# Optimization experiments

Measured on AMD Instinct MI355X. Metric: run time of the kernel, lower is better.

Reference implementation:

```python
import jax, jax.numpy as jnp
import numpy as np

R = 32          # voxel resolution
NORMALIZE = True
EPS = 0.0


def setup_inputs() -> dict:
    key = jax.random.key(0)
    k1, k2 = jax.random.split(key)
    B, N, C = 8, 32768, 64
    features = jax.random.normal(k1, (B, N, C), dtype=jnp.float32)
    coords = jax.random.normal(k2, (B, N, 3), dtype=jnp.float32)
    return {"features": features, "coords": coords}


def _norm_coords(coords):
    # coords: (B, N, 3). Faithful to the torch code: mean over dim 2 (xyz),
    # norm over dim 1 (points), max over dim 2.
    nc = coords - coords.mean(axis=2, keepdims=True)
    if NORMALIZE:
        denom = jnp.max(jnp.linalg.norm(nc, axis=1, keepdims=True), axis=2, keepdims=True) * 2.0 + EPS
        nc = nc / denom + 0.5
    else:
        nc = (nc + 1.0) / 2.0
    return jnp.clip(nc * R, 0, R - 1)


def _avg_voxelize(features, vox_coords):
    B, N, C = features.shape
    R3 = R * R * R
    idx = vox_coords[..., 0] * (R * R) + vox_coords[..., 1] * R + vox_coords[..., 2]  # (B, N)
    flat_idx = (jnp.arange(B, dtype=jnp.int32)[:, None] * R3 + idx).reshape(-1)  # (B*N,)
    sums = jax.ops.segment_sum(features.reshape(B * N, C), flat_idx, num_segments=B * R3)
    counts = jax.ops.segment_sum(jnp.ones((B * N, 1), features.dtype), flat_idx, num_segments=B * R3)
    voxf = sums / jnp.maximum(counts, 1.0)              # (B*R3, C)
    voxf = voxf.reshape(B, R, R, R, C).transpose(0, 4, 1, 2, 3)  # (B, C, R, R, R)
    return voxf


def reference(features, coords):
    nc = _norm_coords(jax.lax.stop_gradient(coords))
    vox_coords = jnp.round(nc).astype(jnp.int32)
    return _avg_voxelize(features, vox_coords), nc
```

## Files before the change

kernel.cpp:

```cpp
#include <hip/hip_runtime.h>
#include <math.h>

#define RR 32
#define R3 (RR*RR*RR)
#define BATCH 8
#define NPTS 32768
#define CCH 64

typedef float vfloat4 __attribute__((ext_vector_type(4)));

static constexpr int SB   = 64;
static constexpr int SBT  = SB * BATCH;
static constexpr int VZB  = 1024;
static constexpr int CZB  = 16;
static constexpr int WPB  = 128;
static constexpr int PPW  = NPTS / WPB;
static constexpr int CHUNK = 64;
static constexpr int NCH  = PPW / CHUNK;

static constexpr size_t OFF_COUNTS   = 0;
static constexpr size_t OFF_PARTIALS = 1u << 20;

__global__ __launch_bounds__(256) void prep_kernel(const float* __restrict__ coords,
                                                   float* __restrict__ voxf,
                                                   int* __restrict__ counts,
                                                   float* __restrict__ partials) {
    int bx = blockIdx.x;
    int tid = threadIdx.x;
    if (bx < SBT) {
        int b = bx >> 6, sb = bx & 63;
        const float* cbase = coords + ((size_t)b * NPTS + sb * (NPTS / SB)) * 3;
        float sx = 0.f, sy = 0.f, sz = 0.f;
        #pragma unroll
        for (int k = 0; k < (NPTS / SB) / 256; ++k) {
            const float* p = cbase + (k * 256 + tid) * 3;
            float x = p[0], y = p[1], z = p[2];
            float m = (x + y + z) * (1.0f / 3.0f);
            float dx = x - m, dy = y - m, dz = z - m;
            sx += dx * dx; sy += dy * dy; sz += dz * dz;
        }
        #pragma unroll
        for (int off = 1; off < 64; off <<= 1) {
            sx += __shfl_xor(sx, off);
            sy += __shfl_xor(sy, off);
            sz += __shfl_xor(sz, off);
        }
        __shared__ float ls[3][4];
        int w = tid >> 6;
        if ((tid & 63) == 0) { ls[0][w] = sx; ls[1][w] = sy; ls[2][w] = sz; }
        __syncthreads();
        if (tid == 0) {
            float* o = partials + (size_t)bx * 3;
            o[0] = ls[0][0] + ls[0][1] + ls[0][2] + ls[0][3];
            o[1] = ls[1][0] + ls[1][1] + ls[1][2] + ls[1][3];
            o[2] = ls[2][0] + ls[2][1] + ls[2][2] + ls[2][3];
        }
        return;
    }
    int zb = bx - SBT;
    vfloat4 z = (vfloat4)(0.f);
    if (zb < VZB) {
        vfloat4* o4 = (vfloat4*)voxf + (size_t)zb * 4096;
        #pragma unroll
        for (int k = 0; k < 16; ++k) o4[k * 256 + tid] = z;
    } else {
        vfloat4* c4 = (vfloat4*)counts + (size_t)(zb - VZB) * 4096;
        #pragma unroll
        for (int k = 0; k < 16; ++k) c4[k * 256 + tid] = z;
    }
}

__global__ __launch_bounds__(256) void feat_kernel(const float* __restrict__ features,
                                                   const float* __restrict__ coords,
                                                   const float* __restrict__ partials,
                                                   float* __restrict__ nc_out,
                                                   int* __restrict__ counts,
                                                   float* __restrict__ voxf) {
    int b = blockIdx.y;
    int tid = threadIdx.x;
    int w = blockIdx.x * 4 + (tid >> 6);
    int lane = tid & 63;
    int sub = lane >> 4;
    int cb  = (lane & 15) << 2;
    const float* fbase = features + (size_t)b * NPTS * CCH;
    const float* crd = coords + (size_t)b * NPTS * 3;
    int* cnt = counts + (size_t)b * R3;
    float* obase = voxf + (size_t)b * CCH * R3;
    int p0 = w * PPW;

    float4 fbuf[2][16];
    #pragma unroll
    for (int i = 0; i < 16; ++i)
        fbuf[0][i] = *(const float4*)(fbase + (size_t)(p0 + i * 4 + sub) * CCH + cb);

    const float* ps = partials + ((size_t)b * SB + lane) * 3;
    float qx = ps[0], qy = ps[1], qz = ps[2];
    #pragma unroll
    for (int off = 1; off < 64; off <<= 1) {
        qx += __shfl_xor(qx, off);
        qy += __shfl_xor(qy, off);
        qz += __shfl_xor(qz, off);
    }
    float mx = fmaxf(fmaxf(sqrtf(qx), sqrtf(qy)), sqrtf(qz));
    float rd = 0.5f / mx;

    float4 acc = make_float4(0.f, 0.f, 0.f, 0.f);
    int curv = -1;
    int nrun = 0;

    auto flushRun = [&]() {
        if (curv < 0) return;
        if (lane == 0) atomicAdd(&cnt[curv], nrun);
        float sx = acc.x, sy = acc.y, sz = acc.z, sw = acc.w;
        sx += __shfl_xor(sx, 16); sx += __shfl_xor(sx, 32);
        sy += __shfl_xor(sy, 16); sy += __shfl_xor(sy, 32);
        sz += __shfl_xor(sz, 16); sz += __shfl_xor(sz, 32);
        sw += __shfl_xor(sw, 16); sw += __shfl_xor(sw, 32);
        float val = (sub == 0) ? sx : (sub == 1) ? sy : (sub == 2) ? sz : sw;
        atomicAdd(&obase[(size_t)(cb + sub) * R3 + curv], val);
    };

    #pragma unroll
    for (int c = 0; c < NCH; ++c) {
        int cur = c & 1;
        if (c + 1 < NCH) {
            #pragma unroll
            for (int i = 0; i < 16; ++i)
                fbuf[cur ^ 1][i] = *(const float4*)(fbase +
                    (size_t)(p0 + (c + 1) * CHUNK + i * 4 + sub) * CCH + cb);
        }
        int pp = p0 + c * CHUNK + lane;
        float x = crd[pp * 3], y = crd[pp * 3 + 1], zz = crd[pp * 3 + 2];
        float m = (x + y + zz) * (1.0f / 3.0f);
        float fx = (x - m) * rd + 0.5f;
        float fy = (y - m) * rd + 0.5f;
        float fz = (zz - m) * rd + 0.5f;
        float tx = fminf(fmaxf(fx * (float)RR, 0.0f), (float)(RR - 1));
        float ty = fminf(fmaxf(fy * (float)RR, 0.0f), (float)(RR - 1));
        float tz = fminf(fmaxf(fz * (float)RR, 0.0f), (float)(RR - 1));
        float* onc = nc_out + (size_t)(b * NPTS + pp) * 3;
        onc[0] = tx; onc[1] = ty; onc[2] = tz;
        int v = (int)rintf(tx) * (RR * RR) + (int)rintf(ty) * RR + (int)rintf(tz);

        int v0 = __shfl(v, 0);
        if (__all(v == v0)) {
            if (v0 != curv) {
                flushRun();
                acc = make_float4(0.f, 0.f, 0.f, 0.f);
                nrun = 0;
                curv = v0;
            }
            #pragma unroll
            for (int i = 0; i < 16; ++i) {
                acc.x += fbuf[cur][i].x; acc.y += fbuf[cur][i].y;
                acc.z += fbuf[cur][i].z; acc.w += fbuf[cur][i].w;
            }
            nrun += CHUNK;
        } else {
            flushRun();
            acc = make_float4(0.f, 0.f, 0.f, 0.f);
            nrun = 0;
            curv = -1;
            atomicAdd(&cnt[v], 1);
            #pragma unroll
            for (int i = 0; i < 16; ++i) {
                int vv = __shfl(v, i * 4 + sub);
                size_t o = (size_t)cb * R3 + vv;
                atomicAdd(&obase[o],          fbuf[cur][i].x);
                atomicAdd(&obase[o + R3],     fbuf[cur][i].y);
                atomicAdd(&obase[o + 2 * R3], fbuf[cur][i].z);
                atomicAdd(&obase[o + 3 * R3], fbuf[cur][i].w);
            }
        }
    }
    flushRun();
}

__global__ __launch_bounds__(256) void scale_kernel(const int* __restrict__ counts,
                                                    float* __restrict__ out) {
    int t = blockIdx.x * 256 + threadIdx.x;
    int lane = threadIdx.x & 63;
    int b = t >> 15;
    int vox = t & (R3 - 1);
    int cnt = counts[t];
    unsigned long long mask = __ballot(cnt > 1);
    while (mask) {
        int src = __ffsll((long long)mask) - 1;
        mask &= mask - 1;
        int vv = __shfl(vox, src);
        int bb = __shfl(b, src);
        int cc = __shfl(cnt, src);
        float s = 1.0f / (float)cc;
        size_t o = ((size_t)bb * CCH + lane) * R3 + vv;
        out[o] *= s;
    }
}

extern "C" void kernel_launch(void* const* d_in, const int* in_sizes, int n_in,
                              void* d_out, int out_size, void* d_ws, size_t ws_size,
                              hipStream_t stream) {
    const float* features = (const float*)d_in[0];
    const float* coords   = (const float*)d_in[1];
    float* out = (float*)d_out;

    float* voxf = out;
    float* nc   = out + (size_t)BATCH * CCH * R3;

    char* ws = (char*)d_ws;
    int*   counts   = (int*)(ws + OFF_COUNTS);
    float* partials = (float*)(ws + OFF_PARTIALS);

    prep_kernel<<<SBT + VZB + CZB, 256, 0, stream>>>(coords, voxf, counts, partials);

    dim3 fgrid(WPB / 4, BATCH);
    feat_kernel<<<fgrid, 256, 0, stream>>>(features, coords, partials, nc, counts, voxf);

    scale_kernel<<<BATCH * R3 / 256, 256, 0, stream>>>(counts, voxf);
}
```

Baseline: 31.82 us.

## Precompute voxel indices and counts so feature scatter applies the mean directly

Splits the pipeline into a stats pass, a per-point pass that writes normalized coords, voxel indices and counts while zeroing the output, and a feature scatter that divides by the final count before each atomic add. This removes the separate scale kernel and its read-modify-write over the output volume, and takes the coordinate math off the feature kernel's path. Feature loads become nontemporal. In exchange the scatter now reads counts for every atomic, adds an index buffer round trip, and still needs three launches.

```diff
diff --git a/kernel.cpp b/kernel.cpp
--- a/kernel.cpp
+++ b/kernel.cpp
@@ -11,8 +11,8 @@
 
 static constexpr int SB   = 64;
 static constexpr int SBT  = SB * BATCH;
+static constexpr int CZB  = 16;
 static constexpr int VZB  = 1024;
-static constexpr int CZB  = 16;
 static constexpr int WPB  = 128;
 static constexpr int PPW  = NPTS / WPB;
 static constexpr int CHUNK = 64;
@@ -20,61 +20,107 @@
 
 static constexpr size_t OFF_COUNTS   = 0;
 static constexpr size_t OFF_PARTIALS = 1u << 20;
-
-__global__ __launch_bounds__(256) void prep_kernel(const float* __restrict__ coords,
-                                                   float* __restrict__ voxf,
-                                                   int* __restrict__ counts,
-                                                   float* __restrict__ partials) {
+static constexpr size_t OFF_IDX      = (1u << 20) + (64u << 10);
+
+__global__ __launch_bounds__(256) void stats_kernel(const float* __restrict__ coords,
+                                                    int* __restrict__ counts,
+                                                    float* __restrict__ partials) {
     int bx = blockIdx.x;
     int tid = threadIdx.x;
-    if (bx < SBT) {
-        int b = bx >> 6, sb = bx & 63;
-        const float* cbase = coords + ((size_t)b * NPTS + sb * (NPTS / SB)) * 3;
-        float sx = 0.f, sy = 0.f, sz = 0.f;
-        #pragma unroll
-        for (int k = 0; k < (NPTS / SB) / 256; ++k) {
-            const float* p = cbase + (k * 256 + tid) * 3;
-            float x = p[0], y = p[1], z = p[2];
-            float m = (x + y + z) * (1.0f / 3.0f);
-            float dx = x - m, dy = y - m, dz = z - m;
-            sx += dx * dx; sy += dy * dy; sz += dz * dz;
-        }
-        #pragma unroll
-        for (int off = 1; off < 64; off <<= 1) {
-            sx += __shfl_xor(sx, off);
-            sy += __shfl_xor(sy, off);
-            sz += __shfl_xor(sz, off);
-        }
-        __shared__ float ls[3][4];
-        int w = tid >> 6;
-        if ((tid & 63) == 0) { ls[0][w] = sx; ls[1][w] = sy; ls[2][w] = sz; }
-        __syncthreads();
-        if (tid == 0) {
-            float* o = partials + (size_t)bx * 3;
-            o[0] = ls[0][0] + ls[0][1] + ls[0][2] + ls[0][3];
-            o[1] = ls[1][0] + ls[1][1] + ls[1][2] + ls[1][3];
-            o[2] = ls[2][0] + ls[2][1] + ls[2][2] + ls[2][3];
-        }
-        return;
-    }
-    int zb = bx - SBT;
-    vfloat4 z = (vfloat4)(0.f);
-    if (zb < VZB) {
-        vfloat4* o4 = (vfloat4*)voxf + (size_t)zb * 4096;
-        #pragma unroll
-        for (int k = 0; k < 16; ++k) o4[k * 256 + tid] = z;
-    } else {
-        vfloat4* c4 = (vfloat4*)counts + (size_t)(zb - VZB) * 4096;
+    if (bx >= SBT) {
+        vfloat4 z = (vfloat4)(0.f);
+        vfloat4* c4 = (vfloat4*)counts + (size_t)(bx - SBT) * 4096;
         #pragma unroll
         for (int k = 0; k < 16; ++k) c4[k * 256 + tid] = z;
+        return;
+    }
+    int b = bx >> 6, sb = bx & 63;
+    const float* cbase = coords + ((size_t)b * NPTS + sb * (NPTS / SB)) * 3;
+    float sx = 0.f, sy = 0.f, sz = 0.f;
+    #pragma unroll
+    for (int k = 0; k < (NPTS / SB) / 256; ++k) {
+        const float* p = cbase + (k * 256 + tid) * 3;
+        float x = p[0], y = p[1], z = p[2];
+        float m = (x + y + z) * (1.0f / 3.0f);
+        float dx = x - m, dy = y - m, dz = z - m;
+        sx += dx * dx; sy += dy * dy; sz += dz * dz;
+    }
+    #pragma unroll
+    for (int off = 1; off < 64; off <<= 1) {
+        sx += __shfl_xor(sx, off);
+        sy += __shfl_xor(sy, off);
+        sz += __shfl_xor(sz, off);
+    }
+    __shared__ float ls[3][4];
+    int w = tid >> 6;
+    if ((tid & 63) == 0) { ls[0][w] = sx; ls[1][w] = sy; ls[2][w] = sz; }
+    __syncthreads();
+    if (tid == 0) {
+        float* o = partials + (size_t)bx * 3;
+        o[0] = ls[0][0] + ls[0][1] + ls[0][2] + ls[0][3];
+        o[1] = ls[1][0] + ls[1][1] + ls[1][2] + ls[1][3];
+        o[2] = ls[2][0] + ls[2][1] + ls[2][2] + ls[2][3];
+    }
+}
+
+__global__ __launch_bounds__(256) void points_kernel(const float* __restrict__ coords,
+                                                     const float* __restrict__ partials,
+                                                     float* __restrict__ voxf,
+                                                     float* __restrict__ nc_out,
+                                                     int* __restrict__ idx_out,
+                                                     int* __restrict__ counts) {
+    int bx = blockIdx.x;
+    int tid = threadIdx.x;
+    int gid = bx * 256 + tid;
+    int b = gid >> 15;
+    int lane = tid & 63;
+
+    float x = coords[(size_t)gid * 3];
+    float y = coords[(size_t)gid * 3 + 1];
+    float zz = coords[(size_t)gid * 3 + 2];
+    const float* ps = partials + ((size_t)b * SB + lane) * 3;
+    float qx = ps[0], qy = ps[1], qz = ps[2];
+
+    {
+        vfloat4 z = (vfloat4)(0.f);
+        vfloat4* o4 = (vfloat4*)voxf + (size_t)bx * 4096;
+        #pragma unroll
+        for (int k = 0; k < 16; ++k)
+            __builtin_nontemporal_store(z, &o4[k * 256 + tid]);
+    }
+
+    #pragma unroll
+    for (int off = 1; off < 64; off <<= 1) {
+        qx += __shfl_xor(qx, off);
+        qy += __shfl_xor(qy, off);
+        qz += __shfl_xor(qz, off);
+    }
+    float mx = fmaxf(fmaxf(sqrtf(qx), sqrtf(qy)), sqrtf(qz));
+    float rd = 0.5f / mx;
+
+    float m = (x + y + zz) * (1.0f / 3.0f);
+    float fx = (x - m) * rd + 0.5f;
+    float fy = (y - m) * rd + 0.5f;
+    float fz = (zz - m) * rd + 0.5f;
+    float tx = fminf(fmaxf(fx * (float)RR, 0.0f), (float)(RR - 1));
+    float ty = fminf(fmaxf(fy * (float)RR, 0.0f), (float)(RR - 1));
+    float tz = fminf(fmaxf(fz * (float)RR, 0.0f), (float)(RR - 1));
+    float* onc = nc_out + (size_t)gid * 3;
+    onc[0] = tx; onc[1] = ty; onc[2] = tz;
+    int v = (int)rintf(tx) * (RR * RR) + (int)rintf(ty) * RR + (int)rintf(tz);
+    idx_out[gid] = v;
+
+    int v0 = __shfl(v, 0);
+    if (__all(v == v0)) {
+        if (lane == 0) atomicAdd(&counts[b * R3 + v0], 64);
+    } else {
+        atomicAdd(&counts[b * R3 + v], 1);
     }
 }
 
 __global__ __launch_bounds__(256) void feat_kernel(const float* __restrict__ features,
-                                                   const float* __restrict__ coords,
-                                                   const float* __restrict__ partials,
-                                                   float* __restrict__ nc_out,
-                                                   int* __restrict__ counts,
+                                                   const int* __restrict__ idx,
+                                                   const int* __restrict__ counts,
                                                    float* __restrict__ voxf) {
     int b = blockIdx.y;
     int tid = threadIdx.x;
@@ -83,41 +129,35 @@
     int sub = lane >> 4;
     int cb  = (lane & 15) << 2;
     const float* fbase = features + (size_t)b * NPTS * CCH;
-    const float* crd = coords + (size_t)b * NPTS * 3;
-    int* cnt = counts + (size_t)b * R3;
+    const int* ibase = idx + (size_t)b * NPTS;
+    const int* cnt = counts + (size_t)b * R3;
     float* obase = voxf + (size_t)b * CCH * R3;
     int p0 = w * PPW;
 
-    float4 fbuf[2][16];
+    int vv[NCH];
+    #pragma unroll
+    for (int c = 0; c < NCH; ++c) vv[c] = ibase[p0 + c * CHUNK + lane];
+
+    vfloat4 fbuf[2][16];
     #pragma unroll
     for (int i = 0; i < 16; ++i)
-        fbuf[0][i] = *(const float4*)(fbase + (size_t)(p0 + i * 4 + sub) * CCH + cb);
-
-    const float* ps = partials + ((size_t)b * SB + lane) * 3;
-    float qx = ps[0], qy = ps[1], qz = ps[2];
-    #pragma unroll
-    for (int off = 1; off < 64; off <<= 1) {
-        qx += __shfl_xor(qx, off);
-        qy += __shfl_xor(qy, off);
-        qz += __shfl_xor(qz, off);
-    }
-    float mx = fmaxf(fmaxf(sqrtf(qx), sqrtf(qy)), sqrtf(qz));
-    float rd = 0.5f / mx;
-
-    float4 acc = make_float4(0.f, 0.f, 0.f, 0.f);
+        fbuf[0][i] = __builtin_nontemporal_load(
+            (const vfloat4*)(fbase + (size_t)(p0 + i * 4 + sub) * CCH + cb));
+
+    vfloat4 acc = (vfloat4)(0.f);
     int curv = -1;
     int nrun = 0;
 
     auto flushRun = [&]() {
         if (curv < 0) return;
-        if (lane == 0) atomicAdd(&cnt[curv], nrun);
         float sx = acc.x, sy = acc.y, sz = acc.z, sw = acc.w;
         sx += __shfl_xor(sx, 16); sx += __shfl_xor(sx, 32);
         sy += __shfl_xor(sy, 16); sy += __shfl_xor(sy, 32);
         sz += __shfl_xor(sz, 16); sz += __shfl_xor(sz, 32);
         sw += __shfl_xor(sw, 16); sw += __shfl_xor(sw, 32);
+        float rc = 1.0f / (float)cnt[curv];
         float val = (sub == 0) ? sx : (sub == 1) ? sy : (sub == 2) ? sz : sw;
-        atomicAdd(&obase[(size_t)(cb + sub) * R3 + curv], val);
+        atomicAdd(&obase[(size_t)(cb + sub) * R3 + curv], val * rc);
     };
 
     #pragma unroll
@@ -126,27 +166,15 @@
         if (c + 1 < NCH) {
             #pragma unroll
             for (int i = 0; i < 16; ++i)
-                fbuf[cur ^ 1][i] = *(const float4*)(fbase +
-                    (size_t)(p0 + (c + 1) * CHUNK + i * 4 + sub) * CCH + cb);
+                fbuf[cur ^ 1][i] = __builtin_nontemporal_load(
+                    (const vfloat4*)(fbase + (size_t)(p0 + (c + 1) * CHUNK + i * 4 + sub) * CCH + cb));
         }
-        int pp = p0 + c * CHUNK + lane;
-        float x = crd[pp * 3], y = crd[pp * 3 + 1], zz = crd[pp * 3 + 2];
-        float m = (x + y + zz) * (1.0f / 3.0f);
-        float fx = (x - m) * rd + 0.5f;
-        float fy = (y - m) * rd + 0.5f;
-        float fz = (zz - m) * rd + 0.5f;
-        float tx = fminf(fmaxf(fx * (float)RR, 0.0f), (float)(RR - 1));
-        float ty = fminf(fmaxf(fy * (float)RR, 0.0f), (float)(RR - 1));
-        float tz = fminf(fmaxf(fz * (float)RR, 0.0f), (float)(RR - 1));
-        float* onc = nc_out + (size_t)(b * NPTS + pp) * 3;
-        onc[0] = tx; onc[1] = ty; onc[2] = tz;
-        int v = (int)rintf(tx) * (RR * RR) + (int)rintf(ty) * RR + (int)rintf(tz);
-
+        int v = vv[c];
         int v0 = __shfl(v, 0);
         if (__all(v == v0)) {
             if (v0 != curv) {
                 flushRun();
-                acc = make_float4(0.f, 0.f, 0.f, 0.f);
+                acc = (vfloat4)(0.f);
                 nrun = 0;
                 curv = v0;
             }
@@ -158,42 +186,22 @@
             nrun += CHUNK;
         } else {
             flushRun();
-            acc = make_float4(0.f, 0.f, 0.f, 0.f);
+            acc = (vfloat4)(0.f);
             nrun = 0;
             curv = -1;
-            atomicAdd(&cnt[v], 1);
             #pragma unroll
             for (int i = 0; i < 16; ++i) {
-                int vv = __shfl(v, i * 4 + sub);
-                size_t o = (size_t)cb * R3 + vv;
-                atomicAdd(&obase[o],          fbuf[cur][i].x);
-                atomicAdd(&obase[o + R3],     fbuf[cur][i].y);
-                atomicAdd(&obase[o + 2 * R3], fbuf[cur][i].z);
-                atomicAdd(&obase[o + 3 * R3], fbuf[cur][i].w);
+                int pv = __shfl(v, i * 4 + sub);
+                float rc = 1.0f / (float)cnt[pv];
+                size_t o = (size_t)cb * R3 + pv;
+                atomicAdd(&obase[o],          fbuf[cur][i].x * rc);
+                atomicAdd(&obase[o + R3],     fbuf[cur][i].y * rc);
+                atomicAdd(&obase[o + 2 * R3], fbuf[cur][i].z * rc);
+                atomicAdd(&obase[o + 3 * R3], fbuf[cur][i].w * rc);
             }
         }
     }
     flushRun();
-}
-
-__global__ __launch_bounds__(256) void scale_kernel(const int* __restrict__ counts,
-                                                    float* __restrict__ out) {
-    int t = blockIdx.x * 256 + threadIdx.x;
-    int lane = threadIdx.x & 63;
-    int b = t >> 15;
-    int vox = t & (R3 - 1);
-    int cnt = counts[t];
-    unsigned long long mask = __ballot(cnt > 1);
-    while (mask) {
-        int src = __ffsll((long long)mask) - 1;
-        mask &= mask - 1;
-        int vv = __shfl(vox, src);
-        int bb = __shfl(b, src);
-        int cc = __shfl(cnt, src);
-        float s = 1.0f / (float)cc;
-        size_t o = ((size_t)bb * CCH + lane) * R3 + vv;
-        out[o] *= s;
-    }
 }
 
 extern "C" void kernel_launch(void* const* d_in, const int* in_sizes, int n_in,
@@ -209,11 +217,12 @@
     char* ws = (char*)d_ws;
     int*   counts   = (int*)(ws + OFF_COUNTS);
     float* partials = (float*)(ws + OFF_PARTIALS);
-
-    prep_kernel<<<SBT + VZB + CZB, 256, 0, stream>>>(coords, voxf, counts, partials);
+    int*   idx      = (int*)(ws + OFF_IDX);
+
+    stats_kernel<<<SBT + CZB, 256, 0, stream>>>(coords, counts, partials);
+
+    points_kernel<<<VZB, 256, 0, stream>>>(coords, partials, voxf, nc, idx, counts);
 
     dim3 fgrid(WPB / 4, BATCH);
-    feat_kernel<<<fgrid, 256, 0, stream>>>(features, coords, partials, nc, counts, voxf);
-
-    scale_kernel<<<BATCH * R3 / 256, 256, 0, stream>>>(counts, voxf);
-}
+    feat_kernel<<<fgrid, 256, 0, stream>>>(features, idx, counts, voxf);
+}
```

New measurement: 39.22 us. 1.23x slower.

## Fuse normalization pass into feature kernel via last-block occupied-voxel list

Applied to the files above, without the earlier changes.

Removes the separate scale kernel. Each thread that is first to increment a voxel's count appends that voxel to a global list. The last block to finish, detected with an atomic ticket counter, walks this list and divides the sums by the counts. This avoids a kernel launch and a full scan of the counts array. In exchange it adds atomics on a shared counter and leaves the final scaling to a single block, which could become serial if many voxels are occupied.

```diff
diff --git a/kernel.cpp b/kernel.cpp
--- a/kernel.cpp
+++ b/kernel.cpp
@@ -17,14 +17,18 @@
 static constexpr int PPW  = NPTS / WPB;
 static constexpr int CHUNK = 64;
 static constexpr int NCH  = PPW / CHUNK;
+static constexpr int FGRID = (WPB / 4) * BATCH;
 
 static constexpr size_t OFF_COUNTS   = 0;
 static constexpr size_t OFF_PARTIALS = 1u << 20;
+static constexpr size_t OFF_CTRL     = (1u << 20) + (64u << 10);
+static constexpr size_t OFF_LIST     = (1u << 20) + (128u << 10);
 
 __global__ __launch_bounds__(256) void prep_kernel(const float* __restrict__ coords,
                                                    float* __restrict__ voxf,
                                                    int* __restrict__ counts,
-                                                   float* __restrict__ partials) {
+                                                   float* __restrict__ partials,
+                                                   int* __restrict__ ctrl) {
     int bx = blockIdx.x;
     int tid = threadIdx.x;
     if (bx < SBT) {
@@ -64,6 +68,7 @@
         #pragma unroll
         for (int k = 0; k < 16; ++k) o4[k * 256 + tid] = z;
     } else {
+        if (zb == VZB && tid < 2) ctrl[tid] = 0;
         vfloat4* c4 = (vfloat4*)counts + (size_t)(zb - VZB) * 4096;
         #pragma unroll
         for (int k = 0; k < 16; ++k) c4[k * 256 + tid] = z;
@@ -75,7 +80,9 @@
                                                    const float* __restrict__ partials,
                                                    float* __restrict__ nc_out,
                                                    int* __restrict__ counts,
-                                                   float* __restrict__ voxf) {
+                                                   float* __restrict__ voxf,
+                                                   int* __restrict__ ctrl,
+                                                   int* __restrict__ list) {
     int b = blockIdx.y;
     int tid = threadIdx.x;
     int w = blockIdx.x * 4 + (tid >> 6);
@@ -110,7 +117,14 @@
 
     auto flushRun = [&]() {
         if (curv < 0) return;
-        if (lane == 0) atomicAdd(&cnt[curv], nrun);
+        if (lane == 0) {
+            int old = atomicAdd(&cnt[curv], nrun);
+            if (old == 0) {
+                int p = atomicAdd(&ctrl[1], 1);
+                __hip_atomic_store(&list[p], (b << 15) | curv,
+                                   __ATOMIC_RELAXED, __HIP_MEMORY_SCOPE_AGENT);
+            }
+        }
         float sx = acc.x, sy = acc.y, sz = acc.z, sw = acc.w;
         sx += __shfl_xor(sx, 16); sx += __shfl_xor(sx, 32);
         sy += __shfl_xor(sy, 16); sy += __shfl_xor(sy, 32);
@@ -161,7 +175,12 @@
             acc = make_float4(0.f, 0.f, 0.f, 0.f);
             nrun = 0;
             curv = -1;
-            atomicAdd(&cnt[v], 1);
+            int old = atomicAdd(&cnt[v], 1);
+            if (old == 0) {
+                int p = atomicAdd(&ctrl[1], 1);
+                __hip_atomic_store(&list[p], (b << 15) | v,
+                                   __ATOMIC_RELAXED, __HIP_MEMORY_SCOPE_AGENT);
+            }
             #pragma unroll
             for (int i = 0; i < 16; ++i) {
                 int vv = __shfl(v, i * 4 + sub);
@@ -174,25 +193,28 @@
         }
     }
     flushRun();
-}
-
-__global__ __launch_bounds__(256) void scale_kernel(const int* __restrict__ counts,
-                                                    float* __restrict__ out) {
-    int t = blockIdx.x * 256 + threadIdx.x;
-    int lane = threadIdx.x & 63;
-    int b = t >> 15;
-    int vox = t & (R3 - 1);
-    int cnt = counts[t];
-    unsigned long long mask = __ballot(cnt > 1);
-    while (mask) {
-        int src = __ffsll((long long)mask) - 1;
-        mask &= mask - 1;
-        int vv = __shfl(vox, src);
-        int bb = __shfl(b, src);
-        int cc = __shfl(cnt, src);
-        float s = 1.0f / (float)cc;
-        size_t o = ((size_t)bb * CCH + lane) * R3 + vv;
-        out[o] *= s;
+
+    __threadfence();
+    __shared__ int sh_last;
+    __syncthreads();
+    if (tid == 0) sh_last = (atomicAdd(&ctrl[0], 1) == FGRID - 1);
+    __syncthreads();
+    if (!sh_last) return;
+    __threadfence();
+    int n = __hip_atomic_load(&ctrl[1], __ATOMIC_RELAXED, __HIP_MEMORY_SCOPE_AGENT);
+    int wv = tid >> 6;
+    for (int e = wv; e < n; e += 4) {
+        int packed = __hip_atomic_load(&list[e], __ATOMIC_RELAXED, __HIP_MEMORY_SCOPE_AGENT);
+        int bb = packed >> 15;
+        int v  = packed & (R3 - 1);
+        int c  = __hip_atomic_load(&counts[(size_t)bb * R3 + v],
+                                   __ATOMIC_RELAXED, __HIP_MEMORY_SCOPE_AGENT);
+        if (c > 1) {
+            float s = 1.0f / (float)c;
+            size_t o = ((size_t)(bb * CCH) + lane) * R3 + v;
+            float curf = __hip_atomic_load(&voxf[o], __ATOMIC_RELAXED, __HIP_MEMORY_SCOPE_AGENT);
+            __hip_atomic_store(&voxf[o], curf * s, __ATOMIC_RELAXED, __HIP_MEMORY_SCOPE_AGENT);
+        }
     }
 }
 
@@ -209,11 +231,12 @@
     char* ws = (char*)d_ws;
     int*   counts   = (int*)(ws + OFF_COUNTS);
     float* partials = (float*)(ws + OFF_PARTIALS);
-
-    prep_kernel<<<SBT + VZB + CZB, 256, 0, stream>>>(coords, voxf, counts, partials);
+    int*   ctrl     = (int*)(ws + OFF_CTRL);
+    int*   list     = (int*)(ws + OFF_LIST);
+
+    prep_kernel<<<SBT + VZB + CZB, 256, 0, stream>>>(coords, voxf, counts, partials, ctrl);
 
     dim3 fgrid(WPB / 4, BATCH);
-    feat_kernel<<<fgrid, 256, 0, stream>>>(features, coords, partials, nc, counts, voxf);
-
-    scale_kernel<<<BATCH * R3 / 256, 256, 0, stream>>>(counts, voxf);
+    feat_kernel<<<fgrid, 256, 0, stream>>>(features, coords, partials, nc, counts,
+                                           voxf, ctrl, list);
 }
```

New measurement: 47.98 us. 1.51x slower.
